# Performance work log

Measured on AMD Instinct MI355X. Metric: run time of the kernel, lower is better.

## Reference

```python
import jax, jax.numpy as jnp
import numpy as np

N = 500_000          # number of tree nodes
K = 8                # attributes per group
ROWS, COLS = 2048, 4096   # image size; P = ROWS*COLS pixels


def _build_euler_tour(n, seed=0):
    """Random tree (parent[i] < i, parent[0] = 0) + real DFS Euler tour with a
    single timer incremented on both entry (tpre) and exit (tpost)."""
    rng = np.random.default_rng(seed)
    parent = np.zeros(n, dtype=np.int64)
    if n > 1:
        parent[1:] = np.floor(rng.random(n - 1) * np.arange(1, n)).astype(np.int64)
    counts = np.bincount(parent[1:], minlength=n)
    starts = np.zeros(n, dtype=np.int64)
    starts[1:] = np.cumsum(counts)[:-1]
    child_order = np.argsort(parent[1:], kind='stable') + 1  # children grouped by parent
    tpre = np.empty(n, dtype=np.int64)
    tpost = np.empty(n, dtype=np.int64)
    next_child = starts.copy()
    ends = starts + counts
    stack = np.empty(n, dtype=np.int64)
    sp = 0
    stack[0] = 0
    timer = 0
    tpre[0] = timer; timer += 1
    while sp >= 0:
        u = stack[sp]
        if next_child[u] < ends[u]:
            v = child_order[next_child[u]]
            next_child[u] += 1
            sp += 1
            stack[sp] = v
            tpre[v] = timer; timer += 1
        else:
            tpost[u] = timer; timer += 1
            sp -= 1
    return tpre, tpost


def setup_inputs() -> dict:
    key = jax.random.key(0)
    k1, k2, k3, k4 = jax.random.split(key, 4)
    tpre_np, tpost_np = _build_euler_tour(N)
    weight = jax.random.normal(k1, (K,), dtype=jnp.float32) * 0.1
    bias = jnp.zeros((1,), dtype=jnp.float32)
    residues = jax.random.normal(k2, (N,), dtype=jnp.float32)
    attrs2d = jax.random.uniform(k3, (N, K), dtype=jnp.float32)
    node_of_pixel = jax.random.randint(k4, (ROWS * COLS,), 0, N)
    return {
        'weight': weight,
        'bias': bias,
        'residues': residues,
        'attrs2d': attrs2d,
        'tpre': jnp.asarray(tpre_np),
        'tpost': jnp.asarray(tpost_np),
        'node_of_pixel': node_of_pixel,
        'numRows': ROWS,
        'numCols': COLS,
    }


def reference(weight, bias, residues, attrs2d, tpre, tpost, node_of_pixel, numRows, numCols):
    beta_f = 1.0  # module default; clamp_logits=False
    # logits = attrs2d @ w + b ; filtered residues per node
    logits = attrs2d @ weight + bias[0]                     # (N,)
    sig = jax.nn.sigmoid(beta_f * logits)                   # (N,)
    filtered = residues * sig                                # (N,)
    # implicit J.T @ filtered via Euler-tour scatter + prefix scan
    T = 2 * tpre.shape[0]                                    # tpost.max()+1 for a full DFS tour
    delta = (jnp.zeros((T,), dtype=filtered.dtype)
             .at[tpre].add(filtered)
             .at[tpost].add(-filtered))
    y_cumsum = jnp.cumsum(delta)                             # (2N,)
    y = y_cumsum[tpre[node_of_pixel]]                        # (P,) gather per pixel
    return y.reshape(numRows, numCols)
```

## Files before the change

### kernel.cpp

```cpp
#include <hip/hip_runtime.h>

typedef int   v4i __attribute__((ext_vector_type(4)));
typedef float v4f __attribute__((ext_vector_type(4)));

#define SCAN_THREADS 256
#define EPT 8
#define CHUNK (SCAN_THREADS * EPT)

#define PSEG     4096
#define PTHREADS 256
#define PPT      16

__global__ void k1_pair_scatter(const float* __restrict__ attrs,
                                const float* __restrict__ weight,
                                const float* __restrict__ bias,
                                const float* __restrict__ residues,
                                const int* __restrict__ tpre,
                                const int* __restrict__ tpost,
                                int2* __restrict__ pairs, int N) {
    int u0 = (blockIdx.x * blockDim.x + threadIdx.x) * 2;
    v4f w0 = *(const v4f*)weight;
    v4f w1 = *(const v4f*)(weight + 4);
    float b = bias[0];
    if (u0 + 2 <= N) {
        float r0 = residues[u0], r1 = residues[u0 + 1];
        int pre0 = tpre[u0],  pre1 = tpre[u0 + 1];
        int pos0 = tpost[u0], pos1 = tpost[u0 + 1];
        v4f a00 = *(const v4f*)(attrs + (size_t)u0 * 8);
        v4f a01 = *(const v4f*)(attrs + (size_t)u0 * 8 + 4);
        v4f a10 = *(const v4f*)(attrs + (size_t)u0 * 8 + 8);
        v4f a11 = *(const v4f*)(attrs + (size_t)u0 * 8 + 12);
        float l0 = a00.x*w0.x + a00.y*w0.y + a00.z*w0.z + a00.w*w0.w +
                   a01.x*w1.x + a01.y*w1.y + a01.z*w1.z + a01.w*w1.w + b;
        float l1 = a10.x*w0.x + a10.y*w0.y + a10.z*w0.z + a10.w*w0.w +
                   a11.x*w1.x + a11.y*w1.y + a11.z*w1.z + a11.w*w1.w + b;
        float f0 = r0 / (1.0f + __expf(-l0));
        float f1 = r1 / (1.0f + __expf(-l1));
        pairs[pre0] = { __float_as_int(f0),  u0 };
        pairs[pre1] = { __float_as_int(f1),  u0 + 1 };
        pairs[pos0] = { __float_as_int(-f0), ~u0 };
        pairs[pos1] = { __float_as_int(-f1), ~(u0 + 1) };
    } else {
        for (int u = u0; u < N; ++u) {
            float logit = b;
            #pragma unroll
            for (int k = 0; k < 8; ++k) logit += attrs[(size_t)u * 8 + k] * weight[k];
            float f = residues[u] / (1.0f + __expf(-logit));
            pairs[tpre[u]]  = { __float_as_int(f),  u };
            pairs[tpost[u]] = { __float_as_int(-f), ~u };
        }
    }
}

__global__ void __launch_bounds__(PTHREADS)
scan_pairs(const int* __restrict__ pairs,
           float* __restrict__ vnode,
           unsigned long long* __restrict__ state, int T) {
    __shared__ float wavesums[PTHREADS / 64];
    __shared__ float s_carry;
    const int seg  = blockIdx.x;
    const int lane = threadIdx.x & 63, wid = threadIdx.x >> 6;
    const int tbase = seg * PSEG + threadIdx.x * PPT;

    float f[PPT]; int idx[PPT];
    #pragma unroll
    for (int j = 0; j < PPT; j += 2) {
        int p = tbase + j;
        if (p + 2 <= T) {
            v4i q = *(const v4i*)(pairs + 2 * (size_t)p);
            f[j]     = __int_as_float(q.x); idx[j]     = q.y;
            f[j + 1] = __int_as_float(q.z); idx[j + 1] = q.w;
        } else {
            #pragma unroll
            for (int k = 0; k < 2; ++k) {
                int pp = p + k;
                if (pp < T) {
                    int2 q = *(const int2*)(pairs + 2 * (size_t)pp);
                    f[j + k] = __int_as_float(q.x); idx[j + k] = q.y;
                } else { f[j + k] = 0.0f; idx[j + k] = -1; }
            }
        }
    }

    float run = 0.0f;
    #pragma unroll
    for (int j = 0; j < PPT; ++j) { run += f[j]; f[j] = run; }

    float x = run;
    #pragma unroll
    for (int d = 1; d < 64; d <<= 1) {
        float y = __shfl_up(x, d, 64);
        if (lane >= d) x += y;
    }
    if (lane == 63) wavesums[wid] = x;
    __syncthreads();
    float woff = 0.0f, agg = 0.0f;
    #pragma unroll
    for (int i = 0; i < PTHREADS / 64; ++i) {
        if (i < wid) woff += wavesums[i];
        agg += wavesums[i];
    }
    float texcl = (x - run) + woff;

    if (threadIdx.x == 0) {
        unsigned long long p = (1ull << 32) |
                               (unsigned long long)__float_as_uint(agg);
        __hip_atomic_store(&state[seg], p, __ATOMIC_RELEASE,
                           __HIP_MEMORY_SCOPE_AGENT);
    }

    if (wid == 0) {
        float c = 0.0f;
        for (int i = lane; i < seg; i += 64) {
            unsigned long long p;
            do {
                p = __hip_atomic_load(&state[i], __ATOMIC_ACQUIRE,
                                      __HIP_MEMORY_SCOPE_AGENT);
            } while ((unsigned)(p >> 32) != 1u);
            c += __uint_as_float((unsigned)(p & 0xffffffffu));
        }
        #pragma unroll
        for (int d = 32; d > 0; d >>= 1) c += __shfl_down(c, d, 64);
        if (lane == 0) s_carry = c;
    }
    __syncthreads();
    float add = s_carry + texcl;

    #pragma unroll
    for (int j = 0; j < PPT; ++j)
        if (idx[j] >= 0) vnode[idx[j]] = f[j] + add;
}

__global__ void k6_gather(const float* __restrict__ vnode,
                          const int* __restrict__ nop,
                          float* __restrict__ out, int P) {
    int i = (blockIdx.x * blockDim.x + threadIdx.x) * 4;
    if (i + 4 <= P) {
        v4i n = *(const v4i*)(nop + i);
        v4f o = { vnode[n.x], vnode[n.y], vnode[n.z], vnode[n.w] };
        *(v4f*)(out + i) = o;
    } else {
        for (; i < P; ++i) out[i] = vnode[nop[i]];
    }
}

__global__ void k1_filter_scatter(const float* __restrict__ attrs,
                                  const float* __restrict__ weight,
                                  const float* __restrict__ bias,
                                  const float* __restrict__ residues,
                                  const int* __restrict__ tpre,
                                  const int* __restrict__ tpost,
                                  float* __restrict__ delta, int N) {
    int u0 = (blockIdx.x * blockDim.x + threadIdx.x) * 2;
    v4f w0 = *(const v4f*)weight;
    v4f w1 = *(const v4f*)(weight + 4);
    float b = bias[0];
    if (u0 + 2 <= N) {
        float r0 = residues[u0], r1 = residues[u0 + 1];
        int pre0 = tpre[u0],  pre1 = tpre[u0 + 1];
        int pos0 = tpost[u0], pos1 = tpost[u0 + 1];
        v4f a00 = *(const v4f*)(attrs + (size_t)u0 * 8);
        v4f a01 = *(const v4f*)(attrs + (size_t)u0 * 8 + 4);
        v4f a10 = *(const v4f*)(attrs + (size_t)u0 * 8 + 8);
        v4f a11 = *(const v4f*)(attrs + (size_t)u0 * 8 + 12);
        float l0 = a00.x*w0.x + a00.y*w0.y + a00.z*w0.z + a00.w*w0.w +
                   a01.x*w1.x + a01.y*w1.y + a01.z*w1.z + a01.w*w1.w + b;
        float l1 = a10.x*w0.x + a10.y*w0.y + a10.z*w0.z + a10.w*w0.w +
                   a11.x*w1.x + a11.y*w1.y + a11.z*w1.z + a11.w*w1.w + b;
        float f0 = r0 / (1.0f + __expf(-l0));
        float f1 = r1 / (1.0f + __expf(-l1));
        delta[pre0] =  f0; delta[pre1] =  f1;
        delta[pos0] = -f0; delta[pos1] = -f1;
    } else {
        for (int u = u0; u < N; ++u) {
            float logit = b;
            #pragma unroll
            for (int k = 0; k < 8; ++k) logit += attrs[(size_t)u * 8 + k] * weight[k];
            float f = residues[u] / (1.0f + __expf(-logit));
            delta[tpre[u]]  =  f;
            delta[tpost[u]] = -f;
        }
    }
}

__global__ void k2_partials(const float* __restrict__ delta,
                            float* __restrict__ partials, int T) {
    __shared__ float sdata[SCAN_THREADS / 64];
    int base = blockIdx.x * CHUNK + threadIdx.x * EPT;
    float s = 0.0f;
    if (base + EPT <= T) {
        v4f v0 = *(const v4f*)(delta + base);
        v4f v1 = *(const v4f*)(delta + base + 4);
        s = v0.x + v0.y + v0.z + v0.w + v1.x + v1.y + v1.z + v1.w;
    } else {
        for (int i = 0; i < EPT; ++i)
            if (base + i < T) s += delta[base + i];
    }
    #pragma unroll
    for (int d = 32; d > 0; d >>= 1) s += __shfl_down(s, d, 64);
    int lane = threadIdx.x & 63, wid = threadIdx.x >> 6;
    if (lane == 0) sdata[wid] = s;
    __syncthreads();
    if (threadIdx.x == 0)
        partials[blockIdx.x] = sdata[0] + sdata[1] + sdata[2] + sdata[3];
}

__global__ void k4_scan_chunks(float* __restrict__ data,
                               const float* __restrict__ partials, int T) {
    __shared__ float wavesums[SCAN_THREADS / 64];
    __shared__ float redsum[SCAN_THREADS / 64];
    int lane = threadIdx.x & 63, wid = threadIdx.x >> 6;
    float c = 0.0f;
    for (int i = threadIdx.x; i < blockIdx.x; i += SCAN_THREADS)
        c += partials[i];
    #pragma unroll
    for (int d = 32; d > 0; d >>= 1) c += __shfl_down(c, d, 64);
    if (lane == 0) redsum[wid] = c;
    int base = blockIdx.x * CHUNK + threadIdx.x * EPT;
    float v[EPT];
    bool full = (base + EPT <= T);
    if (full) {
        v4f v0 = *(const v4f*)(data + base);
        v4f v1 = *(const v4f*)(data + base + 4);
        v[0]=v0.x; v[1]=v0.y; v[2]=v0.z; v[3]=v0.w;
        v[4]=v1.x; v[5]=v1.y; v[6]=v1.z; v[7]=v1.w;
    } else {
        for (int i = 0; i < EPT; ++i)
            v[i] = (base + i < T) ? data[base + i] : 0.0f;
    }
    float run = 0.0f;
    #pragma unroll
    for (int i = 0; i < EPT; ++i) { run += v[i]; v[i] = run; }
    float tot = run;
    float x = tot;
    #pragma unroll
    for (int d = 1; d < 64; d <<= 1) {
        float y = __shfl_up(x, d, 64);
        if (lane >= d) x += y;
    }
    if (lane == 63) wavesums[wid] = x;
    __syncthreads();
    float woff = 0.0f, offset = redsum[0] + redsum[1] + redsum[2] + redsum[3];
    #pragma unroll
    for (int i = 0; i < SCAN_THREADS / 64; ++i)
        if (i < wid) woff += wavesums[i];
    float add = (x - tot) + woff + offset;
    if (full) {
        v4f o0 = { v[0]+add, v[1]+add, v[2]+add, v[3]+add };
        v4f o1 = { v[4]+add, v[5]+add, v[6]+add, v[7]+add };
        *(v4f*)(data + base)     = o0;
        *(v4f*)(data + base + 4) = o1;
    } else {
        for (int i = 0; i < EPT; ++i)
            if (base + i < T) data[base + i] = v[i] + add;
    }
}

__global__ void k5_node_values(const float* __restrict__ ycum,
                               const int* __restrict__ tpre,
                               float* __restrict__ vnode, int N) {
    int u0 = (blockIdx.x * blockDim.x + threadIdx.x) * 2;
    if (u0 + 2 <= N) {
        int t0 = tpre[u0], t1 = tpre[u0 + 1];
        float y0 = ycum[t0], y1 = ycum[t1];
        vnode[u0] = y0; vnode[u0 + 1] = y1;
    } else {
        for (int u = u0; u < N; ++u) vnode[u] = ycum[tpre[u]];
    }
}

extern "C" void kernel_launch(void* const* d_in, const int* in_sizes, int n_in,
                              void* d_out, int out_size, void* d_ws, size_t ws_size,
                              hipStream_t stream) {
    const float* weight   = (const float*)d_in[0];
    const float* bias     = (const float*)d_in[1];
    const float* residues = (const float*)d_in[2];
    const float* attrs    = (const float*)d_in[3];
    const int*   tpre     = (const int*)d_in[4];
    const int*   tpost    = (const int*)d_in[5];
    const int*   nop      = (const int*)d_in[6];
    float* out = (float*)d_out;

    const int N = in_sizes[2];
    const int T = 2 * N;
    const int P = out_size;

    const int numSegs = (T + PSEG - 1) / PSEG;

    size_t needMain = (size_t)N * sizeof(float) + (size_t)numSegs * 8 + 64;
    bool pairsFit = ((size_t)T * sizeof(int2)) <= (size_t)P * sizeof(float);

    if (ws_size >= needMain && pairsFit && numSegs <= 256) {
        float* vnode = (float*)d_ws;
        unsigned long long* state =
            (unsigned long long*)((char*)d_ws + ((size_t)N * 4 + 63) / 64 * 64);
        int2* pairs = (int2*)d_out;
        k1_pair_scatter<<<(N / 2 + 255) / 256, 256, 0, stream>>>(
            attrs, weight, bias, residues, tpre, tpost, pairs, N);
        scan_pairs<<<numSegs, PTHREADS, 0, stream>>>(
            (const int*)pairs, vnode, state, T);
        k6_gather<<<(P / 4 + 255) / 256, 256, 0, stream>>>(vnode, nop, out, P);
    } else {
        const int numChunks = (T + CHUNK - 1) / CHUNK;
        float *delta = out, *vnode = (float*)d_ws, *partials = vnode + N;
        k1_filter_scatter<<<(N / 2 + 255) / 256, 256, 0, stream>>>(
            attrs, weight, bias, residues, tpre, tpost, delta, N);
        k2_partials<<<numChunks, SCAN_THREADS, 0, stream>>>(delta, partials, T);
        k4_scan_chunks<<<numChunks, SCAN_THREADS, 0, stream>>>(delta, partials, T);
        k5_node_values<<<(N / 2 + 255) / 256, 256, 0, stream>>>(delta, tpre, vnode, N);
        k6_gather<<<(P / 4 + 255) / 256, 256, 0, stream>>>(vnode, nop, out, P);
    }
}
```

Measured before the change: 171.9 us.

## Fuse pair scatter and segmented scan into one kernel with spin-wait readiness

Result: slower. 203.7 us (+18.5%).

```diff
diff --git a/kernel.cpp b/kernel.cpp
--- a/kernel.cpp
+++ b/kernel.cpp
@@ -11,75 +11,95 @@
 #define PTHREADS 256
 #define PPT      16
 
-__global__ void k1_pair_scatter(const float* __restrict__ attrs,
-                                const float* __restrict__ weight,
-                                const float* __restrict__ bias,
-                                const float* __restrict__ residues,
-                                const int* __restrict__ tpre,
-                                const int* __restrict__ tpost,
-                                int2* __restrict__ pairs, int N) {
-    int u0 = (blockIdx.x * blockDim.x + threadIdx.x) * 2;
-    v4f w0 = *(const v4f*)weight;
-    v4f w1 = *(const v4f*)(weight + 4);
-    float b = bias[0];
-    if (u0 + 2 <= N) {
-        float r0 = residues[u0], r1 = residues[u0 + 1];
-        int pre0 = tpre[u0],  pre1 = tpre[u0 + 1];
-        int pos0 = tpost[u0], pos1 = tpost[u0 + 1];
-        v4f a00 = *(const v4f*)(attrs + (size_t)u0 * 8);
-        v4f a01 = *(const v4f*)(attrs + (size_t)u0 * 8 + 4);
-        v4f a10 = *(const v4f*)(attrs + (size_t)u0 * 8 + 8);
-        v4f a11 = *(const v4f*)(attrs + (size_t)u0 * 8 + 12);
-        float l0 = a00.x*w0.x + a00.y*w0.y + a00.z*w0.z + a00.w*w0.w +
-                   a01.x*w1.x + a01.y*w1.y + a01.z*w1.z + a01.w*w1.w + b;
-        float l1 = a10.x*w0.x + a10.y*w0.y + a10.z*w0.z + a10.w*w0.w +
-                   a11.x*w1.x + a11.y*w1.y + a11.z*w1.z + a11.w*w1.w + b;
-        float f0 = r0 / (1.0f + __expf(-l0));
-        float f1 = r1 / (1.0f + __expf(-l1));
-        pairs[pre0] = { __float_as_int(f0),  u0 };
-        pairs[pre1] = { __float_as_int(f1),  u0 + 1 };
-        pairs[pos0] = { __float_as_int(-f0), ~u0 };
-        pairs[pos1] = { __float_as_int(-f1), ~(u0 + 1) };
-    } else {
-        for (int u = u0; u < N; ++u) {
-            float logit = b;
-            #pragma unroll
-            for (int k = 0; k < 8; ++k) logit += attrs[(size_t)u * 8 + k] * weight[k];
-            float f = residues[u] / (1.0f + __expf(-logit));
-            pairs[tpre[u]]  = { __float_as_int(f),  u };
-            pairs[tpost[u]] = { __float_as_int(-f), ~u };
-        }
-    }
+__device__ __forceinline__ unsigned long long pack_pair(float f, int j) {
+    return ((unsigned long long)(unsigned)j << 32) |
+           (unsigned long long)__float_as_uint(f);
+}
+__device__ __forceinline__ bool pair_invalid(unsigned long long v) {
+    unsigned j = (unsigned)(v >> 32);
+    return (j == 0u) | (j == 0xAAAAAAAAu);
 }
 
 __global__ void __launch_bounds__(PTHREADS)
-scan_pairs(const int* __restrict__ pairs,
-           float* __restrict__ vnode,
-           unsigned long long* __restrict__ state, int T) {
+fused_scatter_scan(const float* __restrict__ attrs,
+                   const float* __restrict__ weight,
+                   const float* __restrict__ bias,
+                   const float* __restrict__ residues,
+                   const int* __restrict__ tpre,
+                   const int* __restrict__ tpost,
+                   unsigned long long* __restrict__ pairs,
+                   float* __restrict__ vnode,
+                   unsigned long long* __restrict__ state,
+                   int N, int T, int numSegs) {
     __shared__ float wavesums[PTHREADS / 64];
     __shared__ float s_carry;
-    const int seg  = blockIdx.x;
     const int lane = threadIdx.x & 63, wid = threadIdx.x >> 6;
-    const int tbase = seg * PSEG + threadIdx.x * PPT;
-
-    float f[PPT]; int idx[PPT];
-    #pragma unroll
-    for (int j = 0; j < PPT; j += 2) {
-        int p = tbase + j;
-        if (p + 2 <= T) {
-            v4i q = *(const v4i*)(pairs + 2 * (size_t)p);
-            f[j]     = __int_as_float(q.x); idx[j]     = q.y;
-            f[j + 1] = __int_as_float(q.z); idx[j + 1] = q.w;
+
+    {
+        int u0 = (blockIdx.x * PTHREADS + threadIdx.x) * 2;
+        if (u0 + 2 <= N) {
+            v4f w0 = *(const v4f*)weight;
+            v4f w1 = *(const v4f*)(weight + 4);
+            float b = bias[0];
+            float r0 = residues[u0], r1 = residues[u0 + 1];
+            int pre0 = tpre[u0],  pre1 = tpre[u0 + 1];
+            int pos0 = tpost[u0], pos1 = tpost[u0 + 1];
+            v4f a00 = *(const v4f*)(attrs + (size_t)u0 * 8);
+            v4f a01 = *(const v4f*)(attrs + (size_t)u0 * 8 + 4);
+            v4f a10 = *(const v4f*)(attrs + (size_t)u0 * 8 + 8);
+            v4f a11 = *(const v4f*)(attrs + (size_t)u0 * 8 + 12);
+            float l0 = a00.x*w0.x + a00.y*w0.y + a00.z*w0.z + a00.w*w0.w +
+                       a01.x*w1.x + a01.y*w1.y + a01.z*w1.z + a01.w*w1.w + b;
+            float l1 = a10.x*w0.x + a10.y*w0.y + a10.z*w0.z + a10.w*w0.w +
+                       a11.x*w1.x + a11.y*w1.y + a11.z*w1.z + a11.w*w1.w + b;
+            float f0 = r0 / (1.0f + __expf(-l0));
+            float f1 = r1 / (1.0f + __expf(-l1));
+            __hip_atomic_store(&pairs[pre0], pack_pair(f0, u0 + 1),
+                               __ATOMIC_RELAXED, __HIP_MEMORY_SCOPE_AGENT);
+            __hip_atomic_store(&pairs[pre1], pack_pair(f1, u0 + 2),
+                               __ATOMIC_RELAXED, __HIP_MEMORY_SCOPE_AGENT);
+            __hip_atomic_store(&pairs[pos0], pack_pair(-f0, -(u0 + 1)),
+                               __ATOMIC_RELAXED, __HIP_MEMORY_SCOPE_AGENT);
+            __hip_atomic_store(&pairs[pos1], pack_pair(-f1, -(u0 + 2)),
+                               __ATOMIC_RELAXED, __HIP_MEMORY_SCOPE_AGENT);
         } else {
-            #pragma unroll
-            for (int k = 0; k < 2; ++k) {
-                int pp = p + k;
-                if (pp < T) {
-                    int2 q = *(const int2*)(pairs + 2 * (size_t)pp);
-                    f[j + k] = __int_as_float(q.x); idx[j + k] = q.y;
-                } else { f[j + k] = 0.0f; idx[j + k] = -1; }
+            for (int u = u0; u < N; ++u) {
+                float logit = bias[0];
+                #pragma unroll
+                for (int k = 0; k < 8; ++k)
+                    logit += attrs[(size_t)u * 8 + k] * weight[k];
+                float f = residues[u] / (1.0f + __expf(-logit));
+                __hip_atomic_store(&pairs[tpre[u]], pack_pair(f, u + 1),
+                                   __ATOMIC_RELAXED, __HIP_MEMORY_SCOPE_AGENT);
+                __hip_atomic_store(&pairs[tpost[u]], pack_pair(-f, -(u + 1)),
+                                   __ATOMIC_RELAXED, __HIP_MEMORY_SCOPE_AGENT);
             }
         }
+    }
+
+    const int seg = blockIdx.x;
+    if (seg >= numSegs) return;
+    const int tbase = seg * PSEG + threadIdx.x * PPT;
+
+    float f[PPT]; int idx[PPT];
+    unsigned long long v[PPT];
+    #pragma unroll
+    for (int j = 0; j < PPT; ++j) {
+        int p = tbase + j;
+        v[j] = (p < T) ? __hip_atomic_load(&pairs[p], __ATOMIC_RELAXED,
+                                           __HIP_MEMORY_SCOPE_AGENT)
+                       : pack_pair(0.0f, 1);
+    }
+    #pragma unroll
+    for (int j = 0; j < PPT; ++j) {
+        int p = tbase + j;
+        if (p < T) {
+            while (pair_invalid(v[j]))
+                v[j] = __hip_atomic_load(&pairs[p], __ATOMIC_RELAXED,
+                                         __HIP_MEMORY_SCOPE_AGENT);
+            f[j] = __uint_as_float((unsigned)(v[j] & 0xffffffffu));
+            idx[j] = (int)(v[j] >> 32);
+        } else { f[j] = 0.0f; idx[j] = -1; }
     }
 
     float run = 0.0f;
@@ -128,7 +148,7 @@
 
     #pragma unroll
     for (int j = 0; j < PPT; ++j)
-        if (idx[j] >= 0) vnode[idx[j]] = f[j] + add;
+        if (idx[j] > 0) vnode[idx[j] - 1] = f[j] + add;
 }
 
 __global__ void k6_gather(const float* __restrict__ vnode,
@@ -286,19 +306,21 @@
     const int P = out_size;
 
     const int numSegs = (T + PSEG - 1) / PSEG;
-
-    size_t needMain = (size_t)N * sizeof(float) + (size_t)numSegs * 8 + 64;
-    bool pairsFit = ((size_t)T * sizeof(int2)) <= (size_t)P * sizeof(float);
-
-    if (ws_size >= needMain && pairsFit && numSegs <= 256) {
+    const int scatterBlocks = (N / 2 + PTHREADS - 1) / PTHREADS;
+    const int fusedBlocks = max(scatterBlocks, numSegs);
+
+    size_t needMain = (size_t)N * sizeof(float) + (size_t)numSegs * 8 + 128;
+    bool pairsFit = ((size_t)T * 8) <= (size_t)P * sizeof(float);
+    bool coRes = fusedBlocks <= 2048;
+
+    if (ws_size >= needMain && pairsFit && coRes && numSegs <= 256) {
         float* vnode = (float*)d_ws;
         unsigned long long* state =
-            (unsigned long long*)((char*)d_ws + ((size_t)N * 4 + 63) / 64 * 64);
-        int2* pairs = (int2*)d_out;
-        k1_pair_scatter<<<(N / 2 + 255) / 256, 256, 0, stream>>>(
-            attrs, weight, bias, residues, tpre, tpost, pairs, N);
-        scan_pairs<<<numSegs, PTHREADS, 0, stream>>>(
-            (const int*)pairs, vnode, state, T);
+            (unsigned long long*)((char*)d_ws + (((size_t)N * 4 + 127) / 128) * 128);
+        unsigned long long* pairs = (unsigned long long*)d_out;
+        fused_scatter_scan<<<fusedBlocks, PTHREADS, 0, stream>>>(
+            attrs, weight, bias, residues, tpre, tpost, pairs, vnode, state,
+            N, T, numSegs);
         k6_gather<<<(P / 4 + 255) / 256, 256, 0, stream>>>(vnode, nop, out, P);
     } else {
         const int numChunks = (T + CHUNK - 1) / CHUNK;
```
